# Kernel tuning notes

Hardware: AMD Instinct MI355X
Metric: run time of the kernel (lower is better)

Reference implementation:

```python
import math
import jax, jax.numpy as jnp
import numpy as np

# static config (mirrors init_kwargs / input_specs)
B, HRV, WRV, CRV = 2, 32, 1024, 64
CB, HB, WB = 256, 200, 200
D, COUT, HEADS, POINTS = 128, 128, 8, 6
DH = D // HEADS
RMAX = 55.0
XMIN, XMAX, YMIN, YMAX = -50.0, 50.0, -50.0, 50.0


def group_norm(x, gamma, beta, groups, eps=1e-5):
    b, h, w, c = x.shape
    xg = x.reshape(b, h, w, groups, c // groups)
    mean = xg.mean(axis=(1, 2, 4), keepdims=True)
    var = xg.var(axis=(1, 2, 4), keepdims=True)
    xg = (xg - mean) * jax.lax.rsqrt(var + eps)
    return xg.reshape(b, h, w, c) * gamma + beta


def fwd(x_rv, bev, pq_w, pq_b, pv_w, pv_b, po_w, po_b, qs_w1, qs_b1, qs_w2, qs_b2,
        rh_w1, rh_b1, rh_g1, rh_be1, rh_w2, rh_g2, rh_be2, rh_w3, rh_b3,
        so_w, so_b, aw_w, aw_b, vp_w, vp_b, op_w, op_b):
    b = x_rv.shape[0]
    nq = HRV * WRV
    az = jnp.linspace(-math.pi, math.pi, WRV + 1)[:-1]  # [Wrv]
    az = jnp.broadcast_to(az[None, None, :], (b, HRV, WRV))
    coord = jnp.stack([jnp.sin(az), jnp.cos(az), jnp.zeros_like(az)], axis=-1)  # [b,H,W,3]
    Q0 = x_rv @ pq_w + pq_b                                  # 1x1 conv as matmul (NHWC)
    Vmap = bev.transpose(0, 2, 3, 1) @ pv_w + pv_b           # [b,HB,WB,D]
    # range head: 1x1 conv -> GN(8) -> GELU -> 3x3 circular conv -> GN(8) -> GELU -> 1x1 conv
    h = jnp.concatenate([x_rv, coord], axis=-1) @ rh_w1 + rh_b1
    h = jax.nn.gelu(group_norm(h, rh_g1, rh_be1, 8), approximate=False)
    hp = jnp.pad(h, ((0, 0), (1, 1), (1, 1), (0, 0)), mode='wrap')  # circular padding
    h = jax.lax.conv_general_dilated(hp, rh_w2, (1, 1), 'VALID',
                                     dimension_numbers=('NHWC', 'HWIO', 'NHWC'))
    h = jax.nn.gelu(group_norm(h, rh_g2, rh_be2, 8), approximate=False)
    rh = h @ rh_w3 + rh_b3                                   # [b,H,W,2]
    mu = jnp.clip(rh[..., 0], 0.0, RMAX)                     # [b,H,W]
    log_sigma = jnp.clip(rh[..., 1:2], -5.0, 3.0)            # [b,H,W,1]
    sigma = jnp.exp(log_sigma)
    x_mu = mu * jnp.cos(az)
    y_mu = mu * jnp.sin(az)
    rx = jnp.clip((x_mu - XMIN) / (XMAX - XMIN), 0.0, 1.0)
    ry = jnp.clip((y_mu - YMIN) / (YMAX - YMIN), 0.0, 1.0)
    ref = jnp.stack([rx, ry], axis=-1).reshape(b, nq, 2)
    sig_feat = jnp.concatenate([log_sigma, 1.0 / (sigma + 1e-6)], axis=-1)
    q = jnp.concatenate([Q0, sig_feat], axis=-1) @ qs_w1 + qs_b1
    q = jax.nn.gelu(q, approximate=False) @ qs_w2 + qs_b2
    query = q.reshape(b, nq, D)
    # ---- MSDA (num_levels = 1) ----
    value = Vmap.reshape(b, HB * WB, D) @ vp_w + vp_b
    vflat = value.reshape(b, HB * WB, HEADS, DH).transpose(0, 2, 1, 3)  # [b,heads,NV,dh]
    offs = (query @ so_w + so_b).reshape(b, nq, HEADS, POINTS, 2)
    attw = jax.nn.softmax((query @ aw_w + aw_b).reshape(b, nq, HEADS, POINTS), axis=-1)
    norm = jnp.array([WB, HB], dtype=query.dtype)            # offset_normalizer = [W, H]
    loc = ref[:, :, None, None, :] + offs / norm             # [b,nq,heads,P,2] in [0,1]
    loc = loc.transpose(0, 2, 1, 3, 4)                       # [b,heads,nq,P,2]
    attw = attw.transpose(0, 2, 1, 3)                        # [b,heads,nq,P]
    # grid_sample bilinear, zero padding, align_corners=False: pix = loc*size - 0.5
    px = loc[..., 0] * WB - 0.5
    py = loc[..., 1] * HB - 0.5
    x0 = jnp.floor(px).astype(jnp.int32)
    y0 = jnp.floor(py).astype(jnp.int32)
    wx = px - x0
    wy = py - y0

    def gather(xi, yi):
        valid = (xi >= 0) & (xi < WB) & (yi >= 0) & (yi < HB)
        idx = jnp.clip(yi, 0, HB - 1) * WB + jnp.clip(xi, 0, WB - 1)
        g = jnp.take_along_axis(vflat, idx.reshape(b, HEADS, nq * POINTS, 1), axis=2)
        return g.reshape(b, HEADS, nq, POINTS, DH) * valid[..., None]

    sampled = (gather(x0, y0) * ((1 - wx) * (1 - wy))[..., None]
               + gather(x0 + 1, y0) * (wx * (1 - wy))[..., None]
               + gather(x0, y0 + 1) * ((1 - wx) * wy)[..., None]
               + gather(x0 + 1, y0 + 1) * (wx * wy)[..., None])    # [b,heads,nq,P,dh]
    out = (sampled * attw[..., None]).sum(axis=3)                  # [b,heads,nq,dh]
    out = out.transpose(0, 2, 1, 3).reshape(b, nq, D) @ op_w + op_b
    y = out.reshape(b, HRV, WRV, D) @ po_w + po_b                  # proj_o (1x1 conv)
    return y                                                       # [b,Hrv,Wrv,C_out]


def setup_inputs() -> dict:
    key = jax.random.key(0)
    ks = jax.random.split(key, 20)
    def rn(i, shape, s=0.02):
        return s * jax.random.normal(ks[i], shape, jnp.float32)
    z = lambda n: jnp.zeros((n,), jnp.float32)
    o = lambda n: jnp.ones((n,), jnp.float32)
    return dict(
        x_rv=rn(0, (B, HRV, WRV, CRV), 1.0),
        bev=rn(1, (B, CB, HB, WB), 1.0),
        pq_w=rn(2, (CRV, D)), pq_b=z(D),
        pv_w=rn(3, (CB, D)), pv_b=z(D),
        po_w=rn(4, (D, COUT)), po_b=z(COUT),
        qs_w1=rn(5, (D + 2, D)), qs_b1=z(D),
        qs_w2=rn(6, (D, D)), qs_b2=z(D),
        rh_w1=rn(7, (CRV + 3, 128)), rh_b1=z(128),
        rh_g1=o(128), rh_be1=z(128),
        rh_w2=rn(8, (3, 3, 128, 64)),
        rh_g2=o(64), rh_be2=z(64),
        rh_w3=rn(9, (64, 2)), rh_b3=z(2),
        so_w=rn(10, (D, HEADS * POINTS * 2)), so_b=rn(11, (HEADS * POINTS * 2,), 0.5),
        aw_w=rn(12, (D, HEADS * POINTS)), aw_b=z(HEADS * POINTS),
        vp_w=rn(13, (D, D)), vp_b=z(D),
        op_w=rn(14, (D, D)), op_b=z(D),
    )


def reference(x_rv, bev, pq_w, pq_b, pv_w, pv_b, po_w, po_b, qs_w1, qs_b1, qs_w2, qs_b2,
              rh_w1, rh_b1, rh_g1, rh_be1, rh_w2, rh_g2, rh_be2, rh_w3, rh_b3,
              so_w, so_b, aw_w, aw_b, vp_w, vp_b, op_w, op_b):
    return fwd(x_rv, bev, pq_w, pq_b, pv_w, pv_b, po_w, po_b, qs_w1, qs_b1, qs_w2, qs_b2,
               rh_w1, rh_b1, rh_g1, rh_be1, rh_w2, rh_g2, rh_be2, rh_w3, rh_b3,
               so_w, so_b, aw_w, aw_b, vp_w, vp_b, op_w, op_b)
```

## Files before the change

kernel.cpp:

```cpp
#include <hip/hip_runtime.h>
#include <math.h>

#define PI_F 3.14159265358979323846f


typedef __attribute__((ext_vector_type(8))) short bf16x8;
typedef __attribute__((ext_vector_type(4))) float f32x4;

__device__ __forceinline__ float gelu_f(float x) {
    return 0.5f * x * (1.0f + erff(x * 0.70710678118654752440f));
}

__device__ __forceinline__ unsigned short f2bf(float x) {
    unsigned int u = __float_as_uint(x);
    u += 0x7fffu + ((u >> 16) & 1u);
    return (unsigned short)(u >> 16);
}

__device__ __forceinline__ float bf2f(unsigned short h) {
    return __uint_as_float((unsigned int)h << 16);
}

__device__ __forceinline__ size_t fragoff(int k, int c, int KC, int tilebase) {
    return (((size_t)((tilebase + (c >> 4)) * KC + (k >> 5)) * 64) +
            ((k >> 3) & 3) * 16 + (c & 15)) * 8 + (k & 7);
}

__global__ void prep_weights(const float* __restrict__ pv_w, const float* __restrict__ pv_b,
                             const float* __restrict__ vp_w, const float* __restrict__ vp_b,
                             const float* __restrict__ op_w, const float* __restrict__ op_b,
                             const float* __restrict__ po_w, const float* __restrict__ po_b,
                             const float* __restrict__ pq_w, const float* __restrict__ pq_b,
                             const float* __restrict__ qs_w1, const float* __restrict__ qs_b1,
                             const float* __restrict__ qs_w2, const float* __restrict__ qs_b2,
                             const float* __restrict__ so_w, const float* __restrict__ so_b,
                             const float* __restrict__ aw_w, const float* __restrict__ aw_b,
                             const float* __restrict__ rh_w2,
                             unsigned short* __restrict__ wvh, unsigned short* __restrict__ wvl,
                             float* __restrict__ pvvp_b,
                             unsigned short* __restrict__ woh, unsigned short* __restrict__ wol,
                             float* __restrict__ oppo_b,
                             unsigned short* __restrict__ wqh, unsigned short* __restrict__ wql,
                             float* __restrict__ pqqs_b,
                             unsigned short* __restrict__ wah, unsigned short* __restrict__ wal,
                             float* __restrict__ qab,
                             unsigned short* __restrict__ wtb,
                             float2* __restrict__ azsc) {
    int r = blockIdx.x;
    int d = threadIdx.x;
    if (r < 256) {
        float s = 0.f;
        for (int k = 0; k < 128; ++k) s += pv_w[r * 128 + k] * vp_w[k * 128 + d];
        unsigned short h = f2bf(s);
        size_t off = fragoff(r, d, 8, 0);
        wvh[off] = h;
        wvl[off] = f2bf(s - bf2f(h));
    } else if (r == 256) {
        float s = vp_b[d];
        for (int k = 0; k < 128; ++k) s += pv_b[k] * vp_w[k * 128 + d];
        pvvp_b[d] = s;
    } else if (r < 385) {
        int rr = r - 257;
        float s = 0.f;
        for (int k = 0; k < 128; ++k) s += op_w[rr * 128 + k] * po_w[k * 128 + d];
        unsigned short h = f2bf(s);
        size_t off = fragoff(rr, d, 4, 0);
        woh[off] = h;
        wol[off] = f2bf(s - bf2f(h));
    } else if (r == 385) {
        float s = po_b[d];
        for (int k = 0; k < 128; ++k) s += op_b[k] * po_w[k * 128 + d];
        oppo_b[d] = s;
    } else if (r < 450) {
        int rr = r - 386;
        float s = 0.f;
        for (int k = 0; k < 128; ++k) s += pq_w[rr * 128 + k] * qs_w1[k * 128 + d];
        unsigned short h = f2bf(s);
        size_t off = fragoff(rr, d, 2, 0);
        wqh[off] = h;
        wql[off] = f2bf(s - bf2f(h));
    } else if (r == 450) {
        float s = qs_b1[d];
        for (int k = 0; k < 128; ++k) s += pq_b[k] * qs_w1[k * 128 + d];
        pqqs_b[d] = s;
    } else if (r < 459) {
        int w = (r - 451) * 128 + d;
        float az = -PI_F + (float)w * (6.283185307179586f / 1024.0f);
        azsc[w] = make_float2(sinf(az), cosf(az));
    } else if (r < 587) {
        int rr = r - 459;
        if (d < 96) {
            float s = 0.f;
            for (int k = 0; k < 128; ++k) s += qs_w2[rr * 128 + k] * so_w[k * 96 + d];
            unsigned short h = f2bf(s);
            size_t off = fragoff(rr, d, 4, 0);
            wah[off] = h;
            wal[off] = f2bf(s - bf2f(h));
        }
    } else if (r == 587) {
        if (d < 96) {
            float s = so_b[d];
            for (int k = 0; k < 128; ++k) s += qs_b2[k] * so_w[k * 96 + d];
            qab[d] = s;
        }
    } else if (r < 716) {
        int rr = r - 588;
        if (d < 48) {
            float s = 0.f;
            for (int k = 0; k < 128; ++k) s += qs_w2[rr * 128 + k] * aw_w[k * 48 + d];
            unsigned short h = f2bf(s);
            size_t off = fragoff(rr, d, 4, 6);
            wah[off] = h;
            wal[off] = f2bf(s - bf2f(h));
        }
    } else if (r == 716) {
        if (d < 48) {
            float s = aw_b[d];
            for (int k = 0; k < 128; ++k) s += qs_b2[k] * aw_w[k * 48 + d];
            qab[96 + d] = s;
        }
    } else {
        int idx = (r - 717) * 128 + d;
        int ci = idx & 31;
        int o = (idx >> 5) & 63;
        int cc4i = (idx >> 11) & 3;
        int tap = idx >> 13;
        float w = rh_w2[((size_t)tap * 128 + cc4i * 32 + ci) * 64 + o];
        wtb[idx] = f2bf(w);
    }
}

template <int NT, bool STATS>
__global__ __launch_bounds__(2 * NT) void gemm_v3(
    const float* __restrict__ A, int lda,
    const float* __restrict__ W,
    const float* __restrict__ bias,
    float* __restrict__ C, int K,
    const float2* __restrict__ azsc,
    const float* __restrict__ extra2,
    const float* __restrict__ extra_w,
    int emode, int do_gelu, float* __restrict__ stats1) {
    constexpr int NTH = 2 * NT;
    constexpr int NTO = NT / 8;
    __shared__ float As[32][140];
    __shared__ float Ws[32][NT];
    __shared__ float sred[8][2];
    const int tid = threadIdx.x;
    const int tn = tid % NTO;
    const int tm = tid / NTO;
    const int m0 = blockIdx.x * 128;
    if (STATS && tid < 16) sred[tid >> 1][tid & 1] = 0.f;
    float acc[8][8];
#pragma unroll
    for (int i = 0; i < 8; ++i)
#pragma unroll
        for (int j = 0; j < 8; ++j) acc[i][j] = 0.f;

    for (int k0 = 0; k0 < K; k0 += 32) {
        __syncthreads();
        for (int f = tid; f < 1024; f += NTH) {
            int r = f >> 3, c4 = f & 7;
            float4 v = *(const float4*)(A + (size_t)(m0 + r) * lda + k0 + c4 * 4);
            As[c4 * 4 + 0][r] = v.x;
            As[c4 * 4 + 1][r] = v.y;
            As[c4 * 4 + 2][r] = v.z;
            As[c4 * 4 + 3][r] = v.w;
        }
        for (int f = tid; f < 8 * NT; f += NTH) {
            int kk = f / (NT / 4), n4 = f % (NT / 4);
            *(float4*)&Ws[kk][n4 * 4] = *(const float4*)(W + (size_t)(k0 + kk) * NT + n4 * 4);
        }
        __syncthreads();
#pragma unroll 2
        for (int k = 0; k < 32; ++k) {
            const float4 a0 = *(const float4*)&As[k][tm * 8];
            const float4 a1 = *(const float4*)&As[k][tm * 8 + 4];
            const float4 w0 = *(const float4*)&Ws[k][tn * 8];
            const float4 w1 = *(const float4*)&Ws[k][tn * 8 + 4];
            const float av[8] = {a0.x, a0.y, a0.z, a0.w, a1.x, a1.y, a1.z, a1.w};
            const float wv[8] = {w0.x, w0.y, w0.z, w0.w, w1.x, w1.y, w1.z, w1.w};
#pragma unroll
            for (int i = 0; i < 8; ++i)
#pragma unroll
                for (int j = 0; j < 8; ++j) acc[i][j] += av[i] * wv[j];
        }
    }
    float bv[8], e0w[8], e1w[8];
#pragma unroll
    for (int j = 0; j < 8; ++j) bv[j] = bias[tn * 8 + j];
    if (emode) {
#pragma unroll
        for (int j = 0; j < 8; ++j) {
            e0w[j] = extra_w[tn * 8 + j];
            e1w[j] = extra_w[NT + tn * 8 + j];
        }
    }
    float ts = 0.f, ts2 = 0.f;
#pragma unroll
    for (int i = 0; i < 8; ++i) {
        int m = m0 + tm * 8 + i;
        float e0 = 0.f, e1 = 0.f;
        if (emode == 1) {
            float2 sc = azsc[m & 1023];
            e0 = sc.x; e1 = sc.y;
        } else if (emode == 2) {
            e0 = extra2[2 * (size_t)m];
            e1 = extra2[2 * (size_t)m + 1];
        }
        float o[8];
#pragma unroll
        for (int j = 0; j < 8; ++j) {
            float v = acc[i][j] + bv[j];
            if (emode) v += e0 * e0w[j] + e1 * e1w[j];
            if (do_gelu) v = gelu_f(v);
            if (STATS) { ts += v; ts2 += v * v; }
            o[j] = v;
        }
        *(float4*)(C + (size_t)m * NT + tn * 8) = make_float4(o[0], o[1], o[2], o[3]);
        *(float4*)(C + (size_t)m * NT + tn * 8 + 4) = make_float4(o[4], o[5], o[6], o[7]);
    }
    if (STATS) {
        atomicAdd(&sred[tn >> 1][0], ts);
        atomicAdd(&sred[tn >> 1][1], ts2);
        __syncthreads();
        if (tid < 8) {
            int b = m0 >> 15;
            atomicAdd(&stats1[(b * 8 + tid) * 2 + 0], sred[tid][0]);
            atomicAdd(&stats1[(b * 8 + tid) * 2 + 1], sred[tid][1]);
        }
    }
}

template <int KC, int NJ, int EMODE, int GELU, int DUAL>
__global__ __launch_bounds__(256) void gemm_mf(
    const float* __restrict__ A,
    const unsigned short* __restrict__ Bh, const unsigned short* __restrict__ Bl,
    const float* __restrict__ bias,
    float* __restrict__ C1, float* __restrict__ C2,
    const float2* __restrict__ ex2, const float* __restrict__ exw) {
    constexpr int K = KC * 32;
    __shared__ __align__(16) float T0[32 * 70];
    __shared__ __align__(16) float T1[32 * 70];
    const int tid = threadIdx.x;
    const int wid = tid >> 6;
    const int lane = tid & 63;
    const int mm = lane & 15;
    const int quad = lane >> 4;
    const int m0 = blockIdx.x * 64;

    int srow[2], scol[2];
    const float* sp[2];
#pragma unroll
    for (int i = 0; i < 2; ++i) {
        int f = tid + i * 256;
        srow[i] = f >> 3;
        scol[i] = (f & 7) * 4;
        sp[i] = A + (size_t)(m0 + srow[i]) * K + scol[i];
    }

    f32x4 acc[NJ];
#pragma unroll
    for (int j = 0; j < NJ; ++j) acc[j] = (f32x4){0.f, 0.f, 0.f, 0.f};

    union UV { uint4 u; bf16x8 v; };
    float4 st[2];

#define LOADG(K0)                                                 \
    {                                                             \
        _Pragma("unroll")                                         \
        for (int i_ = 0; i_ < 2; ++i_)                            \
            st[i_] = *(const float4*)(sp[i_] + (K0));             \
    }
#define WRITELDS(TB)                                              \
    {                                                             \
        _Pragma("unroll")                                         \
        for (int i_ = 0; i_ < 2; ++i_) {                          \
            _Pragma("unroll")                                     \
            for (int c_ = 0; c_ < 4; ++c_)                        \
                (TB)[(scol[i_] + c_) * 70 + srow[i_]] = st[i_][c_]; \
        }                                                         \
    }
#define BARRIER()                                                 \
    asm volatile("s_waitcnt lgkmcnt(0)" ::: "memory");            \
    __builtin_amdgcn_sched_barrier(0);                            \
    __builtin_amdgcn_s_barrier();                                 \
    __builtin_amdgcn_sched_barrier(0);

    float* Tc = T0;
    float* Tn = T1;
    LOADG(0);
    WRITELDS(Tc);
    if (KC > 1) LOADG(32);
    BARRIER();

#pragma unroll
    for (int t = 0; t < KC; ++t) {
        bf16x8 ah, al;
        {
            const int nc = wid * 16 + mm;
            float f8[8];
#pragma unroll
            for (int jj = 0; jj < 8; ++jj)
                f8[jj] = Tc[(quad * 8 + jj) * 70 + nc];
            unsigned hh[4], ll[4];
#pragma unroll
            for (int q = 0; q < 4; ++q) {
                unsigned u0 = __float_as_uint(f8[2 * q]);
                unsigned u1 = __float_as_uint(f8[2 * q + 1]);
                hh[q] = __builtin_amdgcn_perm(u1, u0, 0x07060302);
                float l0 = f8[2 * q] - __uint_as_float(u0 & 0xffff0000u);
                float l1 = f8[2 * q + 1] - __uint_as_float(u1 & 0xffff0000u);
                asm("v_cvt_pk_bf16_f32 %0, %1, %2" : "=v"(ll[q]) : "v"(l0), "v"(l1));
            }
            UV th, tl;
            th.u = make_uint4(hh[0], hh[1], hh[2], hh[3]);
            tl.u = make_uint4(ll[0], ll[1], ll[2], ll[3]);
            ah = th.v;
            al = tl.v;
        }
        if (t < KC - 1) WRITELDS(Tn);
        if (t < KC - 2) LOADG((t + 2) * 32);
        bf16x8 bh[NJ], bl[NJ];
#pragma unroll
        for (int j = 0; j < NJ; ++j) {
            size_t o = ((size_t)(j * KC + t) * 64 + lane) * 8;
            bh[j] = *(const bf16x8*)(Bh + o);
            bl[j] = *(const bf16x8*)(Bl + o);
        }
#pragma unroll
        for (int j = 0; j < NJ; ++j) {
            acc[j] = __builtin_amdgcn_mfma_f32_16x16x32_bf16(ah, bh[j], acc[j], 0, 0, 0);
            acc[j] = __builtin_amdgcn_mfma_f32_16x16x32_bf16(ah, bl[j], acc[j], 0, 0, 0);
            acc[j] = __builtin_amdgcn_mfma_f32_16x16x32_bf16(al, bh[j], acc[j], 0, 0, 0);
        }
        if (t < KC - 1) {
            BARRIER();
            float* tmp = Tc; Tc = Tn; Tn = tmp;
        }
    }
#undef LOADG
#undef WRITELDS
#undef BARRIER
    float bvj[NJ];
#pragma unroll
    for (int j = 0; j < NJ; ++j) bvj[j] = bias[j * 16 + mm];
    float2 ev[4];
    float e0w[NJ], e1w[NJ];
    if (EMODE) {
#pragma unroll
        for (int r = 0; r < 4; ++r) ev[r] = ex2[m0 + wid * 16 + quad * 4 + r];
#pragma unroll
        for (int j = 0; j < NJ; ++j) {
            e0w[j] = exw[j * 16 + mm];
            e1w[j] = exw[128 + j * 16 + mm];
        }
    }
#pragma unroll
    for (int j = 0; j < NJ; ++j) {
        float* Cp;
        int col, ldc;
        if (DUAL && j >= 6) {
            Cp = C2; col = (j - 6) * 16 + mm; ldc = 48;
        } else {
            Cp = C1; col = j * 16 + mm; ldc = DUAL ? 96 : NJ * 16;
        }
#pragma unroll
        for (int r = 0; r < 4; ++r) {
            int row = m0 + wid * 16 + quad * 4 + r;
            float v = acc[j][r] + bvj[j];
            if (EMODE) v += ev[r].x * e0w[j] + ev[r].y * e1w[j];
            if (GELU) v = gelu_f(v);
            Cp[(size_t)row * ldc + col] = v;
        }
    }
}

__global__ __launch_bounds__(256) void value_gemm_fused(
    const float* __restrict__ bev,
    const unsigned short* __restrict__ Wh, const unsigned short* __restrict__ Wl,
    const float* __restrict__ bf, float* __restrict__ V) {
    __shared__ __align__(16) float T0[32 * 70];
    __shared__ __align__(16) float T1[32 * 70];
    const int tid = threadIdx.x;
    const int wid = tid >> 6;
    const int lane = tid & 63;
    const int m = lane & 15;
    const int quad = lane >> 4;
    const int n0 = blockIdx.x * 64;
    const int b = blockIdx.y;
    const int wn = wid >> 1;
    const int wd = wid & 1;
    const float* src = bev + (size_t)b * 256 * 40000;

    int srow[2], scol[2];
    const float* sp[2];
#pragma unroll
    for (int i = 0; i < 2; ++i) {
        int f = tid + i * 256;
        srow[i] = f >> 4;
        scol[i] = (f & 15) * 4;
        sp[i] = src + n0 + scol[i];
    }

    f32x4 acc[2][4];
#pragma unroll
    for (int i = 0; i < 2; ++i)
#pragma unroll
        for (int j = 0; j < 4; ++j) acc[i][j] = (f32x4){0.f, 0.f, 0.f, 0.f};

    const int dt0 = wd * 4;
    size_t bb[4];
#pragma unroll
    for (int j = 0; j < 4; ++j) bb[j] = (size_t)(dt0 + j) * 4096 + lane * 8;

    union UV { uint4 u; bf16x8 v; };
    float4 st[2];

#define LOADG(K0)                                                           \
    {                                                                       \
        _Pragma("unroll")                                                   \
        for (int i_ = 0; i_ < 2; ++i_)                                      \
            st[i_] = *(const float4*)(sp[i_] + (size_t)((K0) + srow[i_]) * 40000); \
    }
#define WRITELDS(TB)                                                        \
    {                                                                       \
        _Pragma("unroll")                                                   \
        for (int i_ = 0; i_ < 2; ++i_) {                                    \
            float* d_ = (TB) + srow[i_] * 70 + scol[i_];                    \
            *(float2*)(d_ + 0) = make_float2(st[i_].x, st[i_].y);           \
            *(float2*)(d_ + 2) = make_float2(st[i_].z, st[i_].w);           \
        }                                                                   \
    }

    float* Tc = T0;
    float* Tn = T1;
    LOADG(0);
    WRITELDS(Tc);
    LOADG(32);
    asm volatile("s_waitcnt lgkmcnt(0)" ::: "memory");
    __builtin_amdgcn_sched_barrier(0);
    __builtin_amdgcn_s_barrier();
    __builtin_amdgcn_sched_barrier(0);

    for (int t = 0; t < 8; ++t) {
        bf16x8 ah[2], al[2];
#pragma unroll
        for (int i = 0; i < 2; ++i) {
            const int nc = wn * 32 + i * 16 + m;
            float f8[8];
#pragma unroll
            for (int jj = 0; jj < 8; ++jj)
                f8[jj] = Tc[(quad * 8 + jj) * 70 + nc];
            unsigned hh[4], ll[4];
#pragma unroll
            for (int q = 0; q < 4; ++q) {
                unsigned u0 = __float_as_uint(f8[2 * q]);
                unsigned u1 = __float_as_uint(f8[2 * q + 1]);
                hh[q] = __builtin_amdgcn_perm(u1, u0, 0x07060302);
                float l0 = f8[2 * q] - __uint_as_float(u0 & 0xffff0000u);
                float l1 = f8[2 * q + 1] - __uint_as_float(u1 & 0xffff0000u);
                asm("v_cvt_pk_bf16_f32 %0, %1, %2" : "=v"(ll[q]) : "v"(l0), "v"(l1));
            }
            UV th, tl;
            th.u = make_uint4(hh[0], hh[1], hh[2], hh[3]);
            tl.u = make_uint4(ll[0], ll[1], ll[2], ll[3]);
            ah[i] = th.v;
            al[i] = tl.v;
        }
        if (t < 7) WRITELDS(Tn);
        if (t < 6) LOADG(t * 32 + 64);
        bf16x8 bh[4], bl[4];
#pragma unroll
        for (int j = 0; j < 4; ++j) {
            bh[j] = *(const bf16x8*)(Wh + bb[j] + t * 512);
            bl[j] = *(const bf16x8*)(Wl + bb[j] + t * 512);
        }
#pragma unroll
        for (int i = 0; i < 2; ++i)
#pragma unroll
            for (int j = 0; j < 4; ++j) {
                acc[i][j] = __builtin_amdgcn_mfma_f32_16x16x32_bf16(ah[i], bh[j], acc[i][j], 0, 0, 0);
                acc[i][j] = __builtin_amdgcn_mfma_f32_16x16x32_bf16(ah[i], bl[j], acc[i][j], 0, 0, 0);
                acc[i][j] = __builtin_amdgcn_mfma_f32_16x16x32_bf16(al[i], bh[j], acc[i][j], 0, 0, 0);
            }
        if (t < 7) {
            asm volatile("s_waitcnt lgkmcnt(0)" ::: "memory");
            __builtin_amdgcn_sched_barrier(0);
            __builtin_amdgcn_s_barrier();
            __builtin_amdgcn_sched_barrier(0);
            float* tmp = Tc; Tc = Tn; Tn = tmp;
        }
    }
#undef LOADG
#undef WRITELDS
    float bv[4];
#pragma unroll
    for (int j = 0; j < 4; ++j) bv[j] = bf[wd * 64 + j * 16 + m];
#pragma unroll
    for (int i = 0; i < 2; ++i) {
        int nbase = n0 + wn * 32 + i * 16 + quad * 4;
#pragma unroll
        for (int r = 0; r < 4; ++r) {
            int n = nbase + r;
            float* vp = V + ((size_t)b * 40000 + n) * 128 + wd * 64 + m;
#pragma unroll
            for (int j = 0; j < 4; ++j) vp[j * 16] = acc[i][j][r] + bv[j];
        }
    }
}

__global__ __launch_bounds__(256) void gn1_bf16(
    const float* __restrict__ X, const float* __restrict__ stats,
    const float* __restrict__ g1, const float* __restrict__ be1,
    unsigned short* __restrict__ Ob) {
    size_t i4 = (size_t)blockIdx.x * 256 + threadIdx.x;
    size_t base = i4 * 4;
    int c = (int)(base & 127);
    int mrow = (int)(base >> 7);
    int b = mrow >> 15;
    int g = c >> 4;
    float mean = stats[(b * 8 + g) * 2 + 0] * (1.0f / 524288.0f);
    float var = stats[(b * 8 + g) * 2 + 1] * (1.0f / 524288.0f) - mean * mean;
    float rs = 1.0f / sqrtf(var + 1e-5f);
    float4 x = *(const float4*)(X + base);
    float4 gm = *(const float4*)(g1 + c);
    float4 bt = *(const float4*)(be1 + c);
    ushort4 o;
    o.x = f2bf(gelu_f((x.x - mean) * rs * gm.x + bt.x));
    o.y = f2bf(gelu_f((x.y - mean) * rs * gm.y + bt.y));
    o.z = f2bf(gelu_f((x.z - mean) * rs * gm.z + bt.z));
    o.w = f2bf(gelu_f((x.w - mean) * rs * gm.w + bt.w));
    *(ushort4*)(Ob + base) = o;
}

__global__ __launch_bounds__(256, 4) void conv3x3_mfma(
    const unsigned short* __restrict__ H1b,
    const unsigned short* __restrict__ Wtb,
    float* __restrict__ Y,
    float* __restrict__ stats2) {
    __shared__ short As_s[66 * 40];
    __shared__ short Ws_s[3 * 64 * 40];
    __shared__ float sred[8][2];
    const int tid = threadIdx.x;
    const int wid = tid >> 6;
    const int lane = tid & 63;
    const int m = lane & 15;
    const int quad = lane >> 4;
    const int x0 = blockIdx.x * 64;
    const int y = blockIdx.y;
    const int b = blockIdx.z;
    if (tid < 16) sred[tid >> 1][tid & 1] = 0.f;
    f32x4 acc[4];
#pragma unroll
    for (int oq = 0; oq < 4; ++oq) acc[oq] = (f32x4){0.f, 0.f, 0.f, 0.f};

    const unsigned short* Hb = H1b + (size_t)b * 32 * 1024 * 128;
    for (int ry = 0; ry < 3; ++ry) {
        const int gy = (y + ry + 31) & 31;
        const unsigned short* Hrow = Hb + (size_t)gy * 1024 * 128;
        for (int cc4 = 0; cc4 < 4; ++cc4) {
            __syncthreads();
            for (int f = tid; f < 264; f += 256) {
                int xx = f >> 2, cq = f & 3;
                int gx = (x0 + xx + 1023) & 1023;
                uint4 v = *(const uint4*)(Hrow + (size_t)gx * 128 + cc4 * 32 + cq * 8);
                *(uint4*)&As_s[xx * 40 + cq * 8] = v;
            }
            for (int f = tid; f < 768; f += 256) {
                int cq = f & 3, o = (f >> 2) & 63, dx = f >> 8;
                int tap = ry * 3 + dx;
                uint4 v = *(const uint4*)(Wtb + ((size_t)(tap * 4 + cc4) * 64 + o) * 32 + cq * 8);
                *(uint4*)&Ws_s[(dx * 64 + o) * 40 + cq * 8] = v;
            }
            __syncthreads();
            const int arow = wid * 16 + m;
#pragma unroll
            for (int dx = 0; dx < 3; ++dx) {
                bf16x8 a = *(const bf16x8*)&As_s[(arow + dx) * 40 + quad * 8];
#pragma unroll
                for (int oq = 0; oq < 4; ++oq) {
                    bf16x8 bfr = *(const bf16x8*)&Ws_s[(dx * 64 + oq * 16 + m) * 40 + quad * 8];
                    acc[oq] = __builtin_amdgcn_mfma_f32_16x16x32_bf16(a, bfr, acc[oq], 0, 0, 0);
                }
            }
        }
    }
    float sv[4], qv[4];
#pragma unroll
    for (int oq = 0; oq < 4; ++oq) {
        sv[oq] = acc[oq].x + acc[oq].y + acc[oq].z + acc[oq].w;
        qv[oq] = acc[oq].x * acc[oq].x + acc[oq].y * acc[oq].y +
                 acc[oq].z * acc[oq].z + acc[oq].w * acc[oq].w;
    }
    const int masks[5] = {1, 2, 4, 16, 32};
#pragma unroll
    for (int mi = 0; mi < 5; ++mi) {
#pragma unroll
        for (int oq = 0; oq < 4; ++oq) {
            sv[oq] += __shfl_xor(sv[oq], masks[mi]);
            qv[oq] += __shfl_xor(qv[oq], masks[mi]);
        }
    }
    if ((lane & 55) == 0) {
        int gb = (lane >> 3) & 1;
#pragma unroll
        for (int oq = 0; oq < 4; ++oq) {
            atomicAdd(&sred[oq * 2 + gb][0], sv[oq]);
            atomicAdd(&sred[oq * 2 + gb][1], qv[oq]);
        }
    }
    const int pxb = x0 + wid * 16 + quad * 4;
    float* Yb = Y + ((size_t)(b * 32 + y) * 1024 + pxb) * 64;
#pragma unroll
    for (int oq = 0; oq < 4; ++oq) {
        const float av[4] = {acc[oq].x, acc[oq].y, acc[oq].z, acc[oq].w};
#pragma unroll
        for (int r = 0; r < 4; ++r) Yb[(size_t)r * 64 + oq * 16 + m] = av[r];
    }
    __syncthreads();
    if (tid < 16)
        atomicAdd(&stats2[(b * 8 + (tid >> 1)) * 2 + (tid & 1)], sred[tid >> 1][tid & 1]);
}

__global__ __launch_bounds__(256) void rh3_kernel(
    const float* __restrict__ H2, const float* __restrict__ stats,
    const float* __restrict__ gamma, const float* __restrict__ beta, float inv_cnt,
    const float* __restrict__ w3, const float* __restrict__ b3,
    const float2* __restrict__ azsc,
    float2* __restrict__ refxy, float2* __restrict__ sigf) {
    const int tid = threadIdx.x;
    const int lane = tid & 15;
    const int m = blockIdx.x * 16 + (tid >> 4);
    const int b = m >> 15;
    const int c = lane * 4;
    const int g = c >> 3;
    float mean = stats[(b * 8 + g) * 2 + 0] * inv_cnt;
    float var = stats[(b * 8 + g) * 2 + 1] * inv_cnt - mean * mean;
    float rs = 1.0f / sqrtf(var + 1e-5f);
    float4 v = *(const float4*)(H2 + (size_t)m * 64 + c);
    float hv[4];
    hv[0] = gelu_f((v.x - mean) * rs * gamma[c + 0] + beta[c + 0]);
    hv[1] = gelu_f((v.y - mean) * rs * gamma[c + 1] + beta[c + 1]);
    hv[2] = gelu_f((v.z - mean) * rs * gamma[c + 2] + beta[c + 2]);
    hv[3] = gelu_f((v.w - mean) * rs * gamma[c + 3] + beta[c + 3]);
    float d0 = 0.f, d1 = 0.f;
#pragma unroll
    for (int k = 0; k < 4; ++k) {
        d0 += hv[k] * w3[(c + k) * 2 + 0];
        d1 += hv[k] * w3[(c + k) * 2 + 1];
    }
#pragma unroll
    for (int s = 1; s < 16; s <<= 1) {
        d0 += __shfl_xor(d0, s, 16);
        d1 += __shfl_xor(d1, s, 16);
    }
    if (lane == 0) {
        float mu = fminf(fmaxf(d0 + b3[0], 0.f), 55.f);
        float ls = fminf(fmaxf(d1 + b3[1], -5.f), 3.f);
        float sg = expf(ls);
        float2 sc = azsc[m & 1023];
        float rx = fminf(fmaxf(mu * sc.y * 0.01f + 0.5f, 0.f), 1.f);
        float ry = fminf(fmaxf(mu * sc.x * 0.01f + 0.5f, 0.f), 1.f);
        refxy[m] = make_float2(rx, ry);
        sigf[m] = make_float2(ls, 1.f / (sg + 1e-6f));
    }
}

__global__ __launch_bounds__(256) void msda_kernel(
    const float* __restrict__ V, const float2* __restrict__ refxy,
    const float* __restrict__ offs, const float* __restrict__ aw,
    float* __restrict__ out) {
    const int tid = threadIdx.x;
    const int l4 = tid & 3;
    const int grp = tid >> 2;
    const int m = blockIdx.x * 8 + (grp >> 3);
    const int head = grp & 7;
    const int b = m >> 15;
    float2 r = refxy[m];
    const float* lg = aw + (size_t)m * 48 + head * 6;
    float l[6];
#pragma unroll
    for (int p = 0; p < 6; ++p) l[p] = lg[p];
    float mx = l[0];
#pragma unroll
    for (int p = 1; p < 6; ++p) mx = fmaxf(mx, l[p]);
    float s = 0.f;
#pragma unroll
    for (int p = 0; p < 6; ++p) { l[p] = expf(l[p] - mx); s += l[p]; }
    float inv = 1.f / s;
#pragma unroll
    for (int p = 0; p < 6; ++p) l[p] *= inv;
    const float* of = offs + (size_t)m * 96 + head * 12;
    const float* Vb = V + (size_t)b * 40000 * 128 + head * 16 + l4 * 4;
    const float bx = r.x * 200.f - 0.5f;
    const float by = r.y * 200.f - 0.5f;
    f32x4 acc = (f32x4){0.f, 0.f, 0.f, 0.f};
#pragma unroll
    for (int p = 0; p < 6; ++p) {
        float px = bx + of[p * 2 + 0];
        float py = by + of[p * 2 + 1];
        float fx = floorf(px), fy = floorf(py);
        int x0 = (int)fx, y0 = (int)fy;
        float wx = px - fx, wy = py - fy;
        int xc0 = min(max(x0, 0), 199), xc1 = min(max(x0 + 1, 0), 199);
        int yc0 = min(max(y0, 0), 199), yc1 = min(max(y0 + 1, 0), 199);
        bool vx0 = ((unsigned)x0 < 200u), vx1 = ((unsigned)(x0 + 1) < 200u);
        bool vy0 = ((unsigned)y0 < 200u), vy1 = ((unsigned)(y0 + 1) < 200u);
        const f32x4 v00 = *(const f32x4*)(Vb + ((size_t)(yc0 * 200 + xc0)) * 128);
        const f32x4 v10 = *(const f32x4*)(Vb + ((size_t)(yc0 * 200 + xc1)) * 128);
        const f32x4 v01 = *(const f32x4*)(Vb + ((size_t)(yc1 * 200 + xc0)) * 128);
        const f32x4 v11 = *(const f32x4*)(Vb + ((size_t)(yc1 * 200 + xc1)) * 128);
        float w = l[p];
        float w00 = (vx0 && vy0) ? w * (1.f - wx) * (1.f - wy) : 0.f;
        float w10 = (vx1 && vy0) ? w * wx * (1.f - wy) : 0.f;
        float w01 = (vx0 && vy1) ? w * (1.f - wx) * wy : 0.f;
        float w11 = (vx1 && vy1) ? w * wx * wy : 0.f;
        acc += v00 * w00;
        acc += v10 * w10;
        acc += v01 * w01;
        acc += v11 * w11;
    }
    *(f32x4*)(out + (size_t)m * 128 + head * 16 + l4 * 4) = acc;
}

extern "C" void kernel_launch(void* const* d_in, const int* in_sizes, int n_in,
                              void* d_out, int out_size, void* d_ws, size_t ws_size,
                              hipStream_t stream) {
    const float* x_rv = (const float*)d_in[0];
    const float* bev = (const float*)d_in[1];
    const float* pq_w = (const float*)d_in[2];
    const float* pq_b = (const float*)d_in[3];
    const float* pv_w = (const float*)d_in[4];
    const float* pv_b = (const float*)d_in[5];
    const float* po_w = (const float*)d_in[6];
    const float* po_b = (const float*)d_in[7];
    const float* qs_w1 = (const float*)d_in[8];
    const float* qs_b1 = (const float*)d_in[9];
    const float* qs_w2 = (const float*)d_in[10];
    const float* qs_b2 = (const float*)d_in[11];
    const float* rh_w1 = (const float*)d_in[12];
    const float* rh_b1 = (const float*)d_in[13];
    const float* rh_g1 = (const float*)d_in[14];
    const float* rh_be1 = (const float*)d_in[15];
    const float* rh_w2 = (const float*)d_in[16];
    const float* rh_g2 = (const float*)d_in[17];
    const float* rh_be2 = (const float*)d_in[18];
    const float* rh_w3 = (const float*)d_in[19];
    const float* rh_b3 = (const float*)d_in[20];
    const float* so_w = (const float*)d_in[21];
    const float* so_b = (const float*)d_in[22];
    const float* aw_w = (const float*)d_in[23];
    const float* aw_b = (const float*)d_in[24];
    const float* vp_w = (const float*)d_in[25];
    const float* vp_b = (const float*)d_in[26];
    const float* op_w = (const float*)d_in[27];
    const float* op_b = (const float*)d_in[28];

    const int M = 65536;

    float* ws = (float*)d_ws;
    float* azsc = ws;    ws += 2048;
    unsigned short* wvh = (unsigned short*)ws; ws += 16384;
    unsigned short* wvl = (unsigned short*)ws; ws += 16384;
    float* pvvp_b = ws;  ws += 128;
    unsigned short* woh = (unsigned short*)ws; ws += 8192;
    unsigned short* wol = (unsigned short*)ws; ws += 8192;
    float* oppo_b = ws;  ws += 128;
    unsigned short* wqh = (unsigned short*)ws; ws += 4096;
    unsigned short* wql = (unsigned short*)ws; ws += 4096;
    float* pqqs_b = ws;  ws += 128;
    unsigned short* wah = (unsigned short*)ws; ws += 9216;
    unsigned short* wal = (unsigned short*)ws; ws += 9216;
    float* qab = ws;     ws += 144;
    float* stats = ws;   ws += 64;
    unsigned short* wtb = (unsigned short*)ws;  ws += 36864;
    unsigned short* h1b = (unsigned short*)ws;  ws += (size_t)M * 64;
    float* Vv = ws;      ws += (size_t)80000 * 128;
    float* h1 = ws;      ws += (size_t)M * 128;
    float* h2 = ws;      ws += (size_t)M * 64;
    float* q1 = ws;      ws += (size_t)M * 128;
    float* refxy = ws;   ws += (size_t)M * 2;
    float* sigf = ws;    ws += (size_t)M * 2;
    size_t need_bytes = (size_t)(ws - (float*)d_ws) * sizeof(float);
    if (ws_size < need_bytes) return;
    float* offs = h1;
    float* attw = h2;
    float* mo = q1;

    float2* azsc2 = (float2*)azsc;
    float2* refxy2 = (float2*)refxy;
    float2* sigf2 = (float2*)sigf;

    prep_weights<<<1293, 128, 0, stream>>>(
        pv_w, pv_b, vp_w, vp_b, op_w, op_b, po_w, po_b, pq_w, pq_b,
        qs_w1, qs_b1, qs_w2, qs_b2, so_w, so_b, aw_w, aw_b, rh_w2,
        wvh, wvl, pvvp_b, woh, wol, oppo_b, wqh, wql, pqqs_b,
        wah, wal, qab, wtb, azsc2);
    hipMemsetAsync(stats, 0, 64 * sizeof(float), stream);

    value_gemm_fused<<<dim3(625, 2), 256, 0, stream>>>(bev, wvh, wvl, pvvp_b, Vv);

    gemm_v3<128, true><<<M / 128, 256, 0, stream>>>(
        x_rv, 64, rh_w1, rh_b1, h1, 64, azsc2, nullptr, rh_w1 + 64 * 128, 1, 0, stats);

    gn1_bf16<<<8192, 256, 0, stream>>>(h1, stats, rh_g1, rh_be1, h1b);

    conv3x3_mfma<<<dim3(16, 32, 2), 256, 0, stream>>>(h1b, wtb, h2, stats + 32);

    rh3_kernel<<<4096, 256, 0, stream>>>(h2, stats + 32, rh_g2, rh_be2, 1.0f / 262144.0f,
                                         rh_w3, rh_b3, azsc2, refxy2, sigf2);

    gemm_mf<2, 8, 1, 1, 0><<<M / 64, 256, 0, stream>>>(
        x_rv, wqh, wql, pqqs_b, q1, nullptr, sigf2, qs_w1 + 128 * 128);

    gemm_mf<4, 9, 0, 0, 1><<<M / 64, 256, 0, stream>>>(
        q1, wah, wal, qab, offs, attw, nullptr, nullptr);

    msda_kernel<<<M / 8, 256, 0, stream>>>(Vv, refxy2, offs, attw, mo);

    gemm_mf<4, 8, 0, 0, 0><<<M / 64, 256, 0, stream>>>(
        mo, woh, wol, oppo_b, (float*)d_out, nullptr, nullptr, nullptr);
}
```

Measured before the change: 397.1 us.

## Move range-head first GEMM to MFMA and restructure value GEMM per-wave tiles

Replaces the FP32 SIMT gemm_v3 for the range-head 1x1 conv with the MFMA-based gemm_mf path, using split bf16 hi/lo weights and fusing the GroupNorm statistics via wave shuffles and shared atomics. The value GEMM is restructured so that each wave owns 32 rows across all 128 output columns and stages its own private LDS double buffer, removing block-wide barriers at the cost of more registers and accumulators per wave. Tail bounds checks are added because 40000 is not a multiple of 128.

```diff
diff --git a/kernel.cpp b/kernel.cpp
--- a/kernel.cpp
+++ b/kernel.cpp
@@ -35,7 +35,7 @@
                              const float* __restrict__ qs_w2, const float* __restrict__ qs_b2,
                              const float* __restrict__ so_w, const float* __restrict__ so_b,
                              const float* __restrict__ aw_w, const float* __restrict__ aw_b,
-                             const float* __restrict__ rh_w2,
+                             const float* __restrict__ rh_w1, const float* __restrict__ rh_w2,
                              unsigned short* __restrict__ wvh, unsigned short* __restrict__ wvl,
                              float* __restrict__ pvvp_b,
                              unsigned short* __restrict__ woh, unsigned short* __restrict__ wol,
@@ -44,6 +44,7 @@
                              float* __restrict__ pqqs_b,
                              unsigned short* __restrict__ wah, unsigned short* __restrict__ wal,
                              float* __restrict__ qab,
+                             unsigned short* __restrict__ wrh, unsigned short* __restrict__ wrl,
                              unsigned short* __restrict__ wtb,
                              float2* __restrict__ azsc) {
     int r = blockIdx.x;
@@ -119,7 +120,7 @@
             for (int k = 0; k < 128; ++k) s += qs_b2[k] * aw_w[k * 48 + d];
             qab[96 + d] = s;
         }
-    } else {
+    } else if (r < 1293) {
         int idx = (r - 717) * 128 + d;
         int ci = idx & 31;
         int o = (idx >> 5) & 63;
@@ -127,126 +128,35 @@
         int tap = idx >> 13;
         float w = rh_w2[((size_t)tap * 128 + cc4i * 32 + ci) * 64 + o];
         wtb[idx] = f2bf(w);
-    }
-}
-
-template <int NT, bool STATS>
-__global__ __launch_bounds__(2 * NT) void gemm_v3(
-    const float* __restrict__ A, int lda,
-    const float* __restrict__ W,
-    const float* __restrict__ bias,
-    float* __restrict__ C, int K,
-    const float2* __restrict__ azsc,
-    const float* __restrict__ extra2,
-    const float* __restrict__ extra_w,
-    int emode, int do_gelu, float* __restrict__ stats1) {
-    constexpr int NTH = 2 * NT;
-    constexpr int NTO = NT / 8;
-    __shared__ float As[32][140];
-    __shared__ float Ws[32][NT];
-    __shared__ float sred[8][2];
-    const int tid = threadIdx.x;
-    const int tn = tid % NTO;
-    const int tm = tid / NTO;
-    const int m0 = blockIdx.x * 128;
-    if (STATS && tid < 16) sred[tid >> 1][tid & 1] = 0.f;
-    float acc[8][8];
-#pragma unroll
-    for (int i = 0; i < 8; ++i)
-#pragma unroll
-        for (int j = 0; j < 8; ++j) acc[i][j] = 0.f;
-
-    for (int k0 = 0; k0 < K; k0 += 32) {
-        __syncthreads();
-        for (int f = tid; f < 1024; f += NTH) {
-            int r = f >> 3, c4 = f & 7;
-            float4 v = *(const float4*)(A + (size_t)(m0 + r) * lda + k0 + c4 * 4);
-            As[c4 * 4 + 0][r] = v.x;
-            As[c4 * 4 + 1][r] = v.y;
-            As[c4 * 4 + 2][r] = v.z;
-            As[c4 * 4 + 3][r] = v.w;
-        }
-        for (int f = tid; f < 8 * NT; f += NTH) {
-            int kk = f / (NT / 4), n4 = f % (NT / 4);
-            *(float4*)&Ws[kk][n4 * 4] = *(const float4*)(W + (size_t)(k0 + kk) * NT + n4 * 4);
-        }
-        __syncthreads();
-#pragma unroll 2
-        for (int k = 0; k < 32; ++k) {
-            const float4 a0 = *(const float4*)&As[k][tm * 8];
-            const float4 a1 = *(const float4*)&As[k][tm * 8 + 4];
-            const float4 w0 = *(const float4*)&Ws[k][tn * 8];
-            const float4 w1 = *(const float4*)&Ws[k][tn * 8 + 4];
-            const float av[8] = {a0.x, a0.y, a0.z, a0.w, a1.x, a1.y, a1.z, a1.w};
-            const float wv[8] = {w0.x, w0.y, w0.z, w0.w, w1.x, w1.y, w1.z, w1.w};
-#pragma unroll
-            for (int i = 0; i < 8; ++i)
-#pragma unroll
-                for (int j = 0; j < 8; ++j) acc[i][j] += av[i] * wv[j];
-        }
-    }
-    float bv[8], e0w[8], e1w[8];
-#pragma unroll
-    for (int j = 0; j < 8; ++j) bv[j] = bias[tn * 8 + j];
-    if (emode) {
-#pragma unroll
-        for (int j = 0; j < 8; ++j) {
-            e0w[j] = extra_w[tn * 8 + j];
-            e1w[j] = extra_w[NT + tn * 8 + j];
-        }
-    }
-    float ts = 0.f, ts2 = 0.f;
-#pragma unroll
-    for (int i = 0; i < 8; ++i) {
-        int m = m0 + tm * 8 + i;
-        float e0 = 0.f, e1 = 0.f;
-        if (emode == 1) {
-            float2 sc = azsc[m & 1023];
-            e0 = sc.x; e1 = sc.y;
-        } else if (emode == 2) {
-            e0 = extra2[2 * (size_t)m];
-            e1 = extra2[2 * (size_t)m + 1];
-        }
-        float o[8];
-#pragma unroll
-        for (int j = 0; j < 8; ++j) {
-            float v = acc[i][j] + bv[j];
-            if (emode) v += e0 * e0w[j] + e1 * e1w[j];
-            if (do_gelu) v = gelu_f(v);
-            if (STATS) { ts += v; ts2 += v * v; }
-            o[j] = v;
-        }
-        *(float4*)(C + (size_t)m * NT + tn * 8) = make_float4(o[0], o[1], o[2], o[3]);
-        *(float4*)(C + (size_t)m * NT + tn * 8 + 4) = make_float4(o[4], o[5], o[6], o[7]);
-    }
-    if (STATS) {
-        atomicAdd(&sred[tn >> 1][0], ts);
-        atomicAdd(&sred[tn >> 1][1], ts2);
-        __syncthreads();
-        if (tid < 8) {
-            int b = m0 >> 15;
-            atomicAdd(&stats1[(b * 8 + tid) * 2 + 0], sred[tid][0]);
-            atomicAdd(&stats1[(b * 8 + tid) * 2 + 1], sred[tid][1]);
-        }
-    }
-}
-
-template <int KC, int NJ, int EMODE, int GELU, int DUAL>
+    } else {
+        int rr = r - 1293;
+        float w = rh_w1[rr * 128 + d];
+        unsigned short h = f2bf(w);
+        size_t off = fragoff(rr, d, 2, 0);
+        wrh[off] = h;
+        wrl[off] = f2bf(w - bf2f(h));
+    }
+}
+
+template <int KC, int NJ, int EMODE, int GELU, int DUAL, int STATS>
 __global__ __launch_bounds__(256) void gemm_mf(
     const float* __restrict__ A,
     const unsigned short* __restrict__ Bh, const unsigned short* __restrict__ Bl,
     const float* __restrict__ bias,
     float* __restrict__ C1, float* __restrict__ C2,
-    const float2* __restrict__ ex2, const float* __restrict__ exw) {
+    const float2* __restrict__ ex2, const float* __restrict__ exw,
+    float* __restrict__ stats1) {
     constexpr int K = KC * 32;
     __shared__ __align__(16) float T0[32 * 70];
     __shared__ __align__(16) float T1[32 * 70];
+    __shared__ float sred[8][2];
     const int tid = threadIdx.x;
     const int wid = tid >> 6;
     const int lane = tid & 63;
     const int mm = lane & 15;
     const int quad = lane >> 4;
     const int m0 = blockIdx.x * 64;
+    if (STATS && tid < 16) sred[tid >> 1][tid & 1] = 0.f;
 
     int srow[2], scol[2];
     const float* sp[2];
@@ -340,7 +250,6 @@
     }
 #undef LOADG
 #undef WRITELDS
-#undef BARRIER
     float bvj[NJ];
 #pragma unroll
     for (int j = 0; j < NJ; ++j) bvj[j] = bias[j * 16 + mm];
@@ -348,7 +257,10 @@
     float e0w[NJ], e1w[NJ];
     if (EMODE) {
 #pragma unroll
-        for (int r = 0; r < 4; ++r) ev[r] = ex2[m0 + wid * 16 + quad * 4 + r];
+        for (int r = 0; r < 4; ++r) {
+            int row = m0 + wid * 16 + quad * 4 + r;
+            ev[r] = (EMODE == 2) ? ex2[row & 1023] : ex2[row];
+        }
 #pragma unroll
         for (int j = 0; j < NJ; ++j) {
             e0w[j] = exw[j * 16 + mm];
@@ -364,93 +276,108 @@
         } else {
             Cp = C1; col = j * 16 + mm; ldc = DUAL ? 96 : NJ * 16;
         }
+        float tsj = 0.f, t2j = 0.f;
 #pragma unroll
         for (int r = 0; r < 4; ++r) {
             int row = m0 + wid * 16 + quad * 4 + r;
             float v = acc[j][r] + bvj[j];
             if (EMODE) v += ev[r].x * e0w[j] + ev[r].y * e1w[j];
             if (GELU) v = gelu_f(v);
+            if (STATS) { tsj += v; t2j += v * v; }
             Cp[(size_t)row * ldc + col] = v;
         }
-    }
+        if (STATS) {
+#pragma unroll
+            for (int s = 1; s < 64; s <<= 1) {
+                tsj += __shfl_xor(tsj, s);
+                t2j += __shfl_xor(t2j, s);
+            }
+            if (lane == 0) {
+                atomicAdd(&sred[j][0], tsj);
+                atomicAdd(&sred[j][1], t2j);
+            }
+        }
+    }
+    if (STATS) {
+        BARRIER();
+        if (tid < 16) {
+            int b = m0 >> 15;
+            atomicAdd(&stats1[(b * 8 + (tid >> 1)) * 2 + (tid & 1)], sred[tid >> 1][tid & 1]);
+        }
+    }
+#undef BARRIER
 }
 
 __global__ __launch_bounds__(256) void value_gemm_fused(
     const float* __restrict__ bev,
     const unsigned short* __restrict__ Wh, const unsigned short* __restrict__ Wl,
     const float* __restrict__ bf, float* __restrict__ V) {
-    __shared__ __align__(16) float T0[32 * 70];
-    __shared__ __align__(16) float T1[32 * 70];
+    __shared__ __align__(16) float T[4][2][32 * 34];
     const int tid = threadIdx.x;
     const int wid = tid >> 6;
     const int lane = tid & 63;
     const int m = lane & 15;
     const int quad = lane >> 4;
-    const int n0 = blockIdx.x * 64;
+    const int n0 = blockIdx.x * 128 + wid * 32;
     const int b = blockIdx.y;
-    const int wn = wid >> 1;
-    const int wd = wid & 1;
     const float* src = bev + (size_t)b * 256 * 40000;
 
-    int srow[2], scol[2];
-    const float* sp[2];
-#pragma unroll
-    for (int i = 0; i < 2; ++i) {
-        int f = tid + i * 256;
-        srow[i] = f >> 4;
-        scol[i] = (f & 15) * 4;
-        sp[i] = src + n0 + scol[i];
-    }
-
-    f32x4 acc[2][4];
+    int srow[4], scol[4];
+    const float* sp[4];
+#pragma unroll
+    for (int i = 0; i < 4; ++i) {
+        int f = lane + i * 64;
+        srow[i] = f >> 3;
+        scol[i] = (f & 7) * 4;
+        int nl = n0 + scol[i];
+        if (nl > 39996) nl = 39996;
+        sp[i] = src + nl;
+    }
+
+    f32x4 acc[2][8];
 #pragma unroll
     for (int i = 0; i < 2; ++i)
 #pragma unroll
-        for (int j = 0; j < 4; ++j) acc[i][j] = (f32x4){0.f, 0.f, 0.f, 0.f};
-
-    const int dt0 = wd * 4;
-    size_t bb[4];
-#pragma unroll
-    for (int j = 0; j < 4; ++j) bb[j] = (size_t)(dt0 + j) * 4096 + lane * 8;
+        for (int j = 0; j < 8; ++j) acc[i][j] = (f32x4){0.f, 0.f, 0.f, 0.f};
+
+    size_t bb[8];
+#pragma unroll
+    for (int j = 0; j < 8; ++j) bb[j] = (size_t)j * 4096 + lane * 8;
 
     union UV { uint4 u; bf16x8 v; };
-    float4 st[2];
-
-#define LOADG(K0)                                                           \
+    float4 st[4];
+
+#define LOADGV(K0)                                                          \
     {                                                                       \
         _Pragma("unroll")                                                   \
-        for (int i_ = 0; i_ < 2; ++i_)                                      \
+        for (int i_ = 0; i_ < 4; ++i_)                                      \
             st[i_] = *(const float4*)(sp[i_] + (size_t)((K0) + srow[i_]) * 40000); \
     }
-#define WRITELDS(TB)                                                        \
+#define WRITELDSV(TB)                                                       \
     {                                                                       \
         _Pragma("unroll")                                                   \
-        for (int i_ = 0; i_ < 2; ++i_) {                                    \
-            float* d_ = (TB) + srow[i_] * 70 + scol[i_];                    \
+        for (int i_ = 0; i_ < 4; ++i_) {                                    \
+            float* d_ = (TB) + srow[i_] * 34 + scol[i_];                    \
             *(float2*)(d_ + 0) = make_float2(st[i_].x, st[i_].y);           \
             *(float2*)(d_ + 2) = make_float2(st[i_].z, st[i_].w);           \
         }                                                                   \
     }
 
-    float* Tc = T0;
-    float* Tn = T1;
-    LOADG(0);
-    WRITELDS(Tc);
-    LOADG(32);
-    asm volatile("s_waitcnt lgkmcnt(0)" ::: "memory");
-    __builtin_amdgcn_sched_barrier(0);
-    __builtin_amdgcn_s_barrier();
-    __builtin_amdgcn_sched_barrier(0);
-
+    float* Tb0 = &T[wid][0][0];
+    float* Tb1 = &T[wid][1][0];
+    LOADGV(0);
     for (int t = 0; t < 8; ++t) {
+        float* Tc = (t & 1) ? Tb1 : Tb0;
+        WRITELDSV(Tc);
+        if (t < 7) LOADGV((t + 1) * 32);
         bf16x8 ah[2], al[2];
 #pragma unroll
         for (int i = 0; i < 2; ++i) {
-            const int nc = wn * 32 + i * 16 + m;
+            const int nc = i * 16 + m;
             float f8[8];
 #pragma unroll
             for (int jj = 0; jj < 8; ++jj)
-                f8[jj] = Tc[(quad * 8 + jj) * 70 + nc];
+                f8[jj] = Tc[(quad * 8 + jj) * 34 + nc];
             unsigned hh[4], ll[4];
 #pragma unroll
             for (int q = 0; q < 4; ++q) {
@@ -467,44 +394,37 @@
             ah[i] = th.v;
             al[i] = tl.v;
         }
-        if (t < 7) WRITELDS(Tn);
-        if (t < 6) LOADG(t * 32 + 64);
-        bf16x8 bh[4], bl[4];
-#pragma unroll
-        for (int j = 0; j < 4; ++j) {
+        bf16x8 bh[8], bl[8];
+#pragma unroll
+        for (int j = 0; j < 8; ++j) {
             bh[j] = *(const bf16x8*)(Wh + bb[j] + t * 512);
             bl[j] = *(const bf16x8*)(Wl + bb[j] + t * 512);
         }
 #pragma unroll
         for (int i = 0; i < 2; ++i)
 #pragma unroll
-            for (int j = 0; j < 4; ++j) {
+            for (int j = 0; j < 8; ++j) {
                 acc[i][j] = __builtin_amdgcn_mfma_f32_16x16x32_bf16(ah[i], bh[j], acc[i][j], 0, 0, 0);
                 acc[i][j] = __builtin_amdgcn_mfma_f32_16x16x32_bf16(ah[i], bl[j], acc[i][j], 0, 0, 0);
                 acc[i][j] = __builtin_amdgcn_mfma_f32_16x16x32_bf16(al[i], bh[j], acc[i][j], 0, 0, 0);
             }
-        if (t < 7) {
-            asm volatile("s_waitcnt lgkmcnt(0)" ::: "memory");
-            __builtin_amdgcn_sched_barrier(0);
-            __builtin_amdgcn_s_barrier();
-            __builtin_amdgcn_sched_barrier(0);
-            float* tmp = Tc; Tc = Tn; Tn = tmp;
-        }
-    }
-#undef LOADG
-#undef WRITELDS
-    float bv[4];
-#pragma unroll
-    for (int j = 0; j < 4; ++j) bv[j] = bf[wd * 64 + j * 16 + m];
+    }
+#undef LOADGV
+#undef WRITELDSV
+    float bv[8];
+#pragma unroll
+    for (int j = 0; j < 8; ++j) bv[j] = bf[j * 16 + m];
 #pragma unroll
     for (int i = 0; i < 2; ++i) {
-        int nbase = n0 + wn * 32 + i * 16 + quad * 4;
+        int nbase = n0 + i * 16 + quad * 4;
 #pragma unroll
         for (int r = 0; r < 4; ++r) {
             int n = nbase + r;
-            float* vp = V + ((size_t)b * 40000 + n) * 128 + wd * 64 + m;
-#pragma unroll
-            for (int j = 0; j < 4; ++j) vp[j * 16] = acc[i][j][r] + bv[j];
+            if (n < 40000) {
+                float* vp = V + ((size_t)b * 40000 + n) * 128 + m;
+#pragma unroll
+                for (int j = 0; j < 8; ++j) vp[j * 16] = acc[i][j][r] + bv[j];
+            }
         }
     }
 }
@@ -772,6 +692,8 @@
     unsigned short* wah = (unsigned short*)ws; ws += 9216;
     unsigned short* wal = (unsigned short*)ws; ws += 9216;
     float* qab = ws;     ws += 144;
+    unsigned short* wrh = (unsigned short*)ws; ws += 4096;
+    unsigned short* wrl = (unsigned short*)ws; ws += 4096;
     float* stats = ws;   ws += 64;
     unsigned short* wtb = (unsigned short*)ws;  ws += 36864;
     unsigned short* h1b = (unsigned short*)ws;  ws += (size_t)M * 64;
@@ -791,17 +713,17 @@
     float2* refxy2 = (float2*)refxy;
     float2* sigf2 = (float2*)sigf;
 
-    prep_weights<<<1293, 128, 0, stream>>>(
+    prep_weights<<<1357, 128, 0, stream>>>(
         pv_w, pv_b, vp_w, vp_b, op_w, op_b, po_w, po_b, pq_w, pq_b,
-        qs_w1, qs_b1, qs_w2, qs_b2, so_w, so_b, aw_w, aw_b, rh_w2,
+        qs_w1, qs_b1, qs_w2, qs_b2, so_w, so_b, aw_w, aw_b, rh_w1, rh_w2,
         wvh, wvl, pvvp_b, woh, wol, oppo_b, wqh, wql, pqqs_b,
-        wah, wal, qab, wtb, azsc2);
+        wah, wal, qab, wrh, wrl, wtb, azsc2);
     hipMemsetAsync(stats, 0, 64 * sizeof(float), stream);
 
-    value_gemm_fused<<<dim3(625, 2), 256, 0, stream>>>(bev, wvh, wvl, pvvp_b, Vv);
-
-    gemm_v3<128, true><<<M / 128, 256, 0, stream>>>(
-        x_rv, 64, rh_w1, rh_b1, h1, 64, azsc2, nullptr, rh_w1 + 64 * 128, 1, 0, stats);
+    value_gemm_fused<<<dim3(313, 2), 256, 0, stream>>>(bev, wvh, wvl, pvvp_b, Vv);
+
+    gemm_mf<2, 8, 2, 0, 0, 1><<<M / 64, 256, 0, stream>>>(
+        x_rv, wrh, wrl, rh_b1, h1, nullptr, azsc2, rh_w1 + 64 * 128, stats);
 
     gn1_bf16<<<8192, 256, 0, stream>>>(h1, stats, rh_g1, rh_be1, h1b);
 
@@ -810,14 +732,14 @@
     rh3_kernel<<<4096, 256, 0, stream>>>(h2, stats + 32, rh_g2, rh_be2, 1.0f / 262144.0f,
                                          rh_w3, rh_b3, azsc2, refxy2, sigf2);
 
-    gemm_mf<2, 8, 1, 1, 0><<<M / 64, 256, 0, stream>>>(
-        x_rv, wqh, wql, pqqs_b, q1, nullptr, sigf2, qs_w1 + 128 * 128);
-
-    gemm_mf<4, 9, 0, 0, 1><<<M / 64, 256, 0, stream>>>(
-        q1, wah, wal, qab, offs, attw, nullptr, nullptr);
+    gemm_mf<2, 8, 1, 1, 0, 0><<<M / 64, 256, 0, stream>>>(
+        x_rv, wqh, wql, pqqs_b, q1, nullptr, sigf2, qs_w1 + 128 * 128, nullptr);
+
+    gemm_mf<4, 9, 0, 0, 1, 0><<<M / 64, 256, 0, stream>>>(
+        q1, wah, wal, qab, offs, attw, nullptr, nullptr, nullptr);
 
     msda_kernel<<<M / 8, 256, 0, stream>>>(Vv, refxy2, offs, attw, mo);
 
-    gemm_mf<4, 8, 0, 0, 0><<<M / 64, 256, 0, stream>>>(
-        mo, woh, wol, oppo_b, (float*)d_out, nullptr, nullptr, nullptr);
-}
+    gemm_mf<4, 8, 0, 0, 0, 0><<<M / 64, 256, 0, stream>>>(
+        mo, woh, wol, oppo_b, (float*)d_out, nullptr, nullptr, nullptr, nullptr);
+}
```

New measurement: 389.0 us. 2.0% less time.
